# Optimization experiments

Hardware: AMD Instinct MI355X
Metric: run time of the kernel (lower is better)

The kernel has to match this reference:

```python
import jax, jax.numpy as jnp
import numpy as np

N = 3072
F_IN = 512
H1 = 256
HFC = 64
OUT_DIM = 16
NUM_POOL = 3
P_CUT = 30.0  # ps[0]: percentile threshold on positive attention entries
CC_ITERS = 16  # min-label propagation w/ pointer jumping; reach >= 2^16 hops


def l2norm(x):
    # torch F.normalize(p=2, dim=1)
    return x / jnp.clip(jnp.linalg.norm(x, axis=1, keepdims=True), 1e-12, None)


def gcn(x, adj, W, b):
    # standard Kipf GraphConvolution: adj @ (x @ W) + b
    return adj @ (x @ W) + b


def normalize_adj(adj, k):
    n = adj.shape[0]
    A = adj + k * jnp.eye(n, dtype=adj.dtype)
    D = jnp.sqrt(A.sum(0))
    return A / (D[:, None] * D[None, :])


def edge_score(x, adj, a, W, b):
    h = x @ W + b                               # (n, HFC)
    s1 = h @ a[:HFC]                            # (n,)
    s2 = h @ a[HFC:]
    e = jax.nn.sigmoid(s1[:, None] + s2[None, :])
    att = jnp.where(adj > 0, e, jnp.zeros((), e.dtype))
    att = 0.5 * (att + att.T)
    i = jnp.arange(att.shape[0])
    return att.at[i, i].set(1.0)


def percentile_pos(att, p):
    # np.percentile(att[att>0], p) with linear interpolation, jit-safe
    pos = att > 0
    n_pos = pos.sum()
    s = jnp.sort(jnp.where(pos, att, jnp.inf).ravel())
    idx = (n_pos - 1).astype(att.dtype) * (p / 100.0)
    lo = jnp.floor(idx).astype(jnp.int32)
    hi = jnp.ceil(idx).astype(jnp.int32)
    frac = idx - lo.astype(att.dtype)
    return s[lo] * (1.0 - frac) + s[hi] * frac


def cc_labels(mask):
    # connected components via min-label propagation + pointer jumping.
    # diag of mask is always True (att diag = 1), so every node has a neighbor.
    n = mask.shape[0]
    def step(labels, _):
        neigh = jnp.min(jnp.where(mask, labels[None, :], n), axis=1)
        new = jnp.minimum(labels, neigh)
        new = new[new]  # pointer jumping doubles reach each iter
        return new, None
    labels, _ = jax.lax.scan(step, jnp.arange(n, dtype=jnp.int32), None, length=CC_ITERS)
    return labels


def pool(x, adj, att, p):
    cut = percentile_pos(att, p)
    att = att * (att >= cut).astype(att.dtype)
    labels = jax.lax.stop_gradient(cc_labels(att > 0))
    # fixed-shape membership: cluster id = representative (min) node index, padded to N
    C = jax.nn.one_hot(labels, att.shape[0], dtype=x.dtype).T  # (n_clusters=n, n)
    a2 = C @ adj @ C.T
    a2 = 0.5 * (a2 + a2.T)
    cnt = (att > 0).sum(1).astype(x.dtype)  # >=1 since diag survives the cut
    x2 = C @ ((att / cnt[:, None]) @ x)
    return x2, a2, C


def forward(x, adjC, adj, encW0, encb0, encW, encb, fcW, fcb, aW, decW, decb, decW_out, decb_out):
    adjs = [adj]
    adjCs = [adjC]
    xs, Cs, atts = [], [], []
    # ----- encode -----
    for k in range(NUM_POOL):
        x1 = x
        W, b = (encW0, encb0) if k == 0 else (encW[k - 1], encb[k - 1])
        h = jax.nn.relu(gcn(x, adjCs[-1], W, b))
        x = l2norm(h) if k == 0 else l2norm(h + x1)  # residual added for layer idx > 0
        xs.append(x)
        att = edge_score(x, adjs[-1], aW[k], fcW[k], fcb[k])
        x, adjk, C = pool(x, adjs[-1], att, P_CUT)
        adjCk = normalize_adj(adjk, 1.0)  # pool's adjC output is discarded in the original
        x = l2norm(x)
        adjs.append(adjk)
        adjCs.append(adjCk)
        atts.append(att)
        Cs.append(C)
    x = l2norm(jax.nn.elu(gcn(x, adjCs[-1], encW[NUM_POOL - 1], encb[NUM_POOL - 1])))
    xs.append(x)
    # ----- decode -----
    for k in range(NUM_POOL):
        lev = NUM_POOL - k - 1
        x = Cs[lev].T @ x                       # unpool; C is already binary
        x = jnp.concatenate([x, xs[lev]], axis=1)
        x = l2norm(jax.nn.elu(gcn(x, adjCs[lev], decW[k], decb[k])))
    x = gcn(x, adjCs[0], decW_out, decb_out)
    logp = jax.nn.log_softmax(x, axis=1)
    return logp, jnp.stack(Cs), jnp.stack(atts)


def setup_inputs() -> dict:
    key = jax.random.key(0)
    ks = jax.random.split(key, 12)
    x = jax.random.normal(ks[0], (N, F_IN), jnp.float32)
    u = jax.random.uniform(ks[1], (N, N))
    m = (u < 16.0 / N).astype(jnp.float32)  # avg degree ~16
    adj = jnp.maximum(m, m.T)
    i = jnp.arange(N)
    adj = adj.at[i, i].set(1.0)
    adjC = normalize_adj(adj, 1.0)

    def xav(k, shape):
        fan_in = shape[-2] if len(shape) > 1 else shape[-1]
        return jax.random.normal(k, shape, jnp.float32) * (1.0 / np.sqrt(fan_in))

    return {
        "x": x, "adjC": adjC, "adj": adj,
        "encW0": xav(ks[2], (F_IN, H1)), "encb0": jnp.zeros((H1,), jnp.float32),
        "encW": xav(ks[3], (NUM_POOL, H1, H1)), "encb": jnp.zeros((NUM_POOL, H1), jnp.float32),
        "fcW": xav(ks[4], (NUM_POOL, H1, HFC)), "fcb": jnp.zeros((NUM_POOL, HFC), jnp.float32),
        "aW": xav(ks[5], (NUM_POOL, 2 * HFC)),
        "decW": xav(ks[6], (NUM_POOL, 2 * H1, H1)), "decb": jnp.zeros((NUM_POOL, H1), jnp.float32),
        "decW_out": xav(ks[7], (H1, OUT_DIM)), "decb_out": jnp.zeros((OUT_DIM,), jnp.float32),
    }


def reference(x, adjC, adj, encW0, encb0, encW, encb, fcW, fcb, aW, decW, decb, decW_out, decb_out):
    return forward(x, adjC, adj, encW0, encb0, encW, encb, fcW, fcb, aW, decW, decb, decW_out, decb_out)
```

## Files before the change

kernel.cpp:

```cpp
#include <hip/hip_runtime.h>
#include <math.h>

#define NN 3072
#define FF 256
#define CAPE (1<<18)
#define MAXCH 3200

struct Scal {
  int nnzS, nnz2, nzero, mtot, ncht;
  int lo, hi, rank_rem, below_acc, c_le;
  unsigned prefix, vlo, minabove;
  float frac, cut;
};

__device__ __forceinline__ float sigm(float x){ return 1.0f/(1.0f+expf(-x)); }

__global__ __launch_bounds__(256) void k_count_dense(const float* __restrict__ A, int* __restrict__ rowcnt, float* __restrict__ Drow){
  int i=blockIdx.x, t=threadIdx.x;
  int c=0; float sm=0.f;
  for(int j=t;j<NN;j+=256){ float a=A[(size_t)i*NN+j]; if(a!=0.0f||j==i) c++; sm+=a; }
  __shared__ int s[256]; __shared__ float fs[256];
  s[t]=c; fs[t]=sm; __syncthreads();
  for(int o=128;o;o>>=1){ if(t<o){ s[t]+=s[t+o]; fs[t]+=fs[t+o]; } __syncthreads(); }
  if(t==0){ rowcnt[i]=s[0]; if(Drow) Drow[i]=sqrtf(fs[0]+1.0f); }
}

__global__ __launch_bounds__(1024) void k_scan(const int* __restrict__ cnt, int* __restrict__ rp, int* __restrict__ total){
  int t=threadIdx.x;
  int a0=cnt[t*3+0], a1=cnt[t*3+1], a2=cnt[t*3+2];
  int loc=a0+a1+a2;
  __shared__ int s[1024];
  s[t]=loc; __syncthreads();
  for(int o=1;o<1024;o<<=1){ int v=(t>=o)?s[t-o]:0; __syncthreads(); s[t]+=v; __syncthreads(); }
  int excl=s[t]-loc;
  rp[t*3+0]=excl; rp[t*3+1]=excl+a0; rp[t*3+2]=excl+a0+a1;
  if(t==1023){ rp[NN]=s[t]; *total=s[t]; }
}

__global__ __launch_bounds__(256) void k_fill_dense(const float* __restrict__ A, const float* __restrict__ ACd, const float* __restrict__ D,
    const int* __restrict__ rp, int* __restrict__ rows, int* __restrict__ cols, float* __restrict__ aval, float* __restrict__ acval){
  int i=blockIdx.x, t=threadIdx.x;
  const int CH=NN/256;
  int j0=t*CH; int c=0;
  for(int u=0;u<CH;u++){ int j=j0+u; float a=A[(size_t)i*NN+j]; if(a!=0.0f||j==i) c++; }
  __shared__ int s[256]; s[t]=c; __syncthreads();
  for(int o=1;o<256;o<<=1){ int v=(t>=o)?s[t-o]:0; __syncthreads(); s[t]+=v; __syncthreads(); }
  int pos=rp[i]+s[t]-c;
  float Di = D?D[i]:0.0f;
  for(int u=0;u<CH;u++){ int j=j0+u; float a=A[(size_t)i*NN+j];
    if(a!=0.0f||j==i){
      if(pos<CAPE){
        rows[pos]=i; cols[pos]=j; aval[pos]=a;
        acval[pos]= ACd? ACd[(size_t)i*NN+j] : (a+(j==i?1.0f:0.0f))/(Di*D[j]);
      }
      pos++;
    }
  }
}

__global__ __launch_bounds__(256) void k_gemm(const float* __restrict__ A, const float* __restrict__ B, float* __restrict__ C,
                                              int M, int K, int Nc){
  __shared__ float As[16][68];
  __shared__ float Bs[16][68];
  int tid=threadIdx.x;
  int tx=tid&15, ty=tid>>4;
  int bm=blockIdx.y*64, bn=blockIdx.x*64;
  int lm=tid>>2, lk=(tid&3)*4;
  int kr=tid>>4, nf=(tid&15)*4;
  float acc[4][4]={};
  for(int k0=0;k0<K;k0+=16){
    float4 a4=*(const float4*)(A+(size_t)(bm+lm)*K+k0+lk);
    As[lk+0][lm]=a4.x; As[lk+1][lm]=a4.y; As[lk+2][lm]=a4.z; As[lk+3][lm]=a4.w;
    float4 b4=*(const float4*)(B+(size_t)(k0+kr)*Nc+bn+nf);
    *(float4*)&Bs[kr][nf]=b4;
    __syncthreads();
#pragma unroll
    for(int kk=0;kk<16;kk++){
      float4 av=*(const float4*)&As[kk][ty*4];
      float4 bv=*(const float4*)&Bs[kk][tx*4];
      float am[4]={av.x,av.y,av.z,av.w};
      float bb[4]={bv.x,bv.y,bv.z,bv.w};
#pragma unroll
      for(int i2=0;i2<4;i2++)
#pragma unroll
        for(int j2=0;j2<4;j2++) acc[i2][j2]+=am[i2]*bb[j2];
    }
    __syncthreads();
  }
  for(int i2=0;i2<4;i2++){
    float4 o=make_float4(acc[i2][0],acc[i2][1],acc[i2][2],acc[i2][3]);
    *(float4*)(C+(size_t)(bm+ty*4+i2)*Nc+bn+tx*4)=o;
  }
}

__global__ __launch_bounds__(256) void k_gemm16(const float* __restrict__ X, const float* __restrict__ W, float* __restrict__ T){
  int idx=blockIdx.x*256+threadIdx.x;
  if(idx>=NN*16) return;
  int i=idx>>4, o=idx&15;
  float s=0.f;
  for(int kk=0;kk<FF;kk++) s+=X[(size_t)i*FF+kk]*W[kk*16+o];
  T[idx]=s;
}

__global__ __launch_bounds__(256) void k_spmm_gcn(const int* __restrict__ rp, const int* __restrict__ cols, const float* __restrict__ vals,
    const float* __restrict__ X, const float* __restrict__ bias, const float* __restrict__ resid, float* __restrict__ out, int act){
  int wid=blockIdx.x*4+(threadIdx.x>>6);
  int lane=threadIdx.x&63;
  if(wid>=NN) return;
  int e0=rp[wid], e1=rp[wid+1];
  float4 acc=make_float4(0,0,0,0);
  for(int e=e0;e<e1;e++){
    float v=vals[e]; int c=cols[e];
    float4 xv=*(const float4*)(X+(size_t)c*FF+lane*4);
    acc.x+=v*xv.x; acc.y+=v*xv.y; acc.z+=v*xv.z; acc.w+=v*xv.w;
  }
  float4 bv=*(const float4*)(bias+lane*4);
  acc.x+=bv.x; acc.y+=bv.y; acc.z+=bv.z; acc.w+=bv.w;
  if(act==0){
    acc.x=fmaxf(acc.x,0.f); acc.y=fmaxf(acc.y,0.f); acc.z=fmaxf(acc.z,0.f); acc.w=fmaxf(acc.w,0.f);
  } else {
    acc.x=acc.x>0.f?acc.x:expm1f(acc.x); acc.y=acc.y>0.f?acc.y:expm1f(acc.y);
    acc.z=acc.z>0.f?acc.z:expm1f(acc.z); acc.w=acc.w>0.f?acc.w:expm1f(acc.w);
  }
  if(resid){
    float4 r=*(const float4*)(resid+(size_t)wid*FF+lane*4);
    acc.x+=r.x; acc.y+=r.y; acc.z+=r.z; acc.w+=r.w;
  }
  float ss=acc.x*acc.x+acc.y*acc.y+acc.z*acc.z+acc.w*acc.w;
  for(int o=32;o;o>>=1) ss+=__shfl_xor(ss,o);
  float nrm=fmaxf(sqrtf(ss),1e-12f);
  float4 o4=make_float4(acc.x/nrm,acc.y/nrm,acc.z/nrm,acc.w/nrm);
  *(float4*)(out+(size_t)wid*FF+lane*4)=o4;
}

__global__ __launch_bounds__(256) void k_spmm_plain(const int* __restrict__ rp, const int* __restrict__ cols, const float* __restrict__ vals,
    const float* __restrict__ X, float* __restrict__ out){
  int wid=blockIdx.x*4+(threadIdx.x>>6);
  int lane=threadIdx.x&63;
  if(wid>=NN) return;
  int e0=rp[wid], e1=rp[wid+1];
  float4 acc=make_float4(0,0,0,0);
  for(int e=e0;e<e1;e++){
    if(e>=CAPE) break;
    float v=vals[e]; int c=cols[e];
    float4 xv=*(const float4*)(X+(size_t)c*FF+lane*4);
    acc.x+=v*xv.x; acc.y+=v*xv.y; acc.z+=v*xv.z; acc.w+=v*xv.w;
  }
  *(float4*)(out+(size_t)wid*FF+lane*4)=acc;
}

__global__ __launch_bounds__(64) void k_edge(const float* __restrict__ X, const float* __restrict__ fw, const float* __restrict__ fb,
    const float* __restrict__ av, float* __restrict__ s1, float* __restrict__ s2, Scal* sc){
  int i=blockIdx.x, l=threadIdx.x;
  if(i==0&&l==0) sc->nzero=0;
  __shared__ float xr[FF];
  *(float4*)&xr[l*4]=*(const float4*)(X+(size_t)i*FF+l*4);
  __syncthreads();
  float h=fb[l];
  for(int kk=0;kk<FF;kk++) h+=xr[kk]*fw[kk*64+l];
  float p1=h*av[l], p2=h*av[64+l];
  for(int o=32;o;o>>=1){ p1+=__shfl_xor(p1,o); p2+=__shfl_xor(p2,o); }
  if(l==0){ s1[i]=p1; s2[i]=p2; }
}

__global__ __launch_bounds__(256) void k_att_row(const int* __restrict__ rp, const int* __restrict__ cols,
    const float* __restrict__ s1, const float* __restrict__ s2, float* __restrict__ attD, float* __restrict__ cand, Scal* sc){
  __shared__ float row[NN];
  __shared__ int wred[4];
  int i=blockIdx.x, t=threadIdx.x;
  for(int j=t;j<NN;j+=256) row[j]=0.f;
  __syncthreads();
  int e0=rp[i], e1=rp[i+1];
  float s1i=s1[i], s2i=s2[i];
  int nz=0;
  for(int e=e0+t;e<e1;e+=256){
    int j=cols[e];
    float v=(j==i)?1.0f:0.5f*(sigm(s1i+s2[j])+sigm(s1[j]+s2i));
    row[j]=v;
    if(e<CAPE) cand[e]=v;
    if(!(v>0.f)) nz++;
  }
  for(int o=32;o;o>>=1) nz+=__shfl_xor(nz,o);
  if((t&63)==0) wred[t>>6]=nz;
  __syncthreads();
  if(t==0){ int s=wred[0]+wred[1]+wred[2]+wred[3]; if(s) atomicAdd(&sc->nzero,s); }
  float* orow=attD+(size_t)i*NN;
  for(int j=t*4;j<NN;j+=1024) *(float4*)(orow+j)=*(const float4*)&row[j];
}

__global__ void k_prep(Scal* sc){
  int np=sc->nnzS - sc->nzero;
  float idx=(float)(np-1)*(30.0f/100.0f);
  float fl=floorf(idx), ce=ceilf(idx);
  sc->lo=(int)fl; sc->hi=(int)ce; sc->frac=idx-fl;
  sc->rank_rem=sc->lo;
  sc->below_acc=0;
  sc->minabove=0xFFFFFFFFu;
}

template<int PHASE>
__global__ __launch_bounds__(256) void k_hist(const float* __restrict__ cand, const Scal* __restrict__ sc, unsigned* __restrict__ bins){
  const int NB = (PHASE==0)?16384:256;
  __shared__ unsigned h[NB];
  int t=threadIdx.x;
  for(int b=t;b<NB;b+=256) h[b]=0;
  __syncthreads();
  int n=sc->nnzS; if(n>CAPE) n=CAPE;
  unsigned pref=sc->prefix;
  int stride=gridDim.x*256;
  for(int e=blockIdx.x*256+t; e<n; e+=stride){
    float v=cand[e];
    if(!(v>0.f)) continue;
    unsigned bb=__float_as_uint(v);
    if(PHASE==0) atomicAdd(&h[bb>>16],1u);
    else if(PHASE==1){ if((bb>>16)==pref) atomicAdd(&h[(bb>>8)&0xFFu],1u); }
    else { if((bb>>8)==pref) atomicAdd(&h[bb&0xFFu],1u); }
  }
  __syncthreads();
  for(int b=t;b<NB;b+=256){ unsigned c=h[b]; if(c) atomicAdd(&bins[b],c); }
}

template<int PHASE>
__global__ __launch_bounds__(256) void k_pick(const unsigned* __restrict__ bins, Scal* sc){
  const int NB=(PHASE==0)?16384:256;
  const int PER=NB/256;
  __shared__ int part[256];
  __shared__ int selbin; __shared__ int below_sel;
  int t=threadIdx.x;
  int b0=t*PER;
  int sum=0;
  for(int u=0;u<PER;u++) sum+=(int)bins[b0+u];
  part[t]=sum; __syncthreads();
  for(int o=1;o<256;o<<=1){ int v=(t>=o)?part[t-o]:0; __syncthreads(); part[t]+=v; __syncthreads(); }
  int incl=part[t], excl=incl-sum;
  int r=sc->rank_rem;
  if(r>=excl && r<incl){
    int run=excl;
    for(int u=0;u<PER;u++){
      int c=(int)bins[b0+u];
      if(r<run+c){ selbin=b0+u; below_sel=run; break; }
      run+=c;
    }
  }
  __syncthreads();
  if(t==0){
    sc->rank_rem=r-below_sel;
    sc->below_acc+=below_sel;
    if(PHASE==0) sc->prefix=(unsigned)selbin;
    else if(PHASE==1) sc->prefix=(sc->prefix<<8)|(unsigned)selbin;
    else{
      sc->vlo=(sc->prefix<<8)|(unsigned)selbin;
      sc->c_le=sc->below_acc+(int)bins[selbin];
    }
  }
}

__global__ __launch_bounds__(256) void k_minabove(const float* __restrict__ cand, Scal* sc){
  int n=sc->nnzS; if(n>CAPE) n=CAPE;
  unsigned vlo=sc->vlo;
  int tid=threadIdx.x, lane=tid&63;
  int stride=gridDim.x*256;
  for(int base=blockIdx.x*256; base<n; base+=stride){
    int e=base+tid;
    unsigned b=0xFFFFFFFFu;
    if(e<n){ float v=cand[e]; if(v>0.f){ unsigned bb=__float_as_uint(v); if(bb>vlo) b=bb; } }
    for(int o=32;o;o>>=1){ unsigned ob=__shfl_xor(b,o); b=ob<b?ob:b; }
    if(lane==0&&b!=0xFFFFFFFFu) atomicMin(&sc->minabove,b);
  }
}

__global__ void k_cut(Scal* sc){
  float slo=__uint_as_float(sc->vlo);
  float shi;
  if(sc->hi==sc->lo) shi=slo;
  else if(sc->c_le>sc->hi) shi=slo;
  else shi=__uint_as_float(sc->minabove);
  sc->cut=slo*(1.0f-sc->frac)+shi*sc->frac;
}

__global__ __launch_bounds__(256) void k_pc_count(const int* __restrict__ rp, const float* __restrict__ cand, const Scal* __restrict__ sc,
    int* __restrict__ rowcnt, float* __restrict__ cntf){
  int wid=blockIdx.x*4+(threadIdx.x>>6);
  int lane=threadIdx.x&63;
  if(wid>=NN) return;
  int e0=rp[wid], e1=rp[wid+1];
  float cut=sc->cut;
  int c=0;
  for(int e=e0+lane;e<e1;e+=64){ if(e<CAPE && cand[e]>=cut) c++; }
  for(int o=32;o;o>>=1) c+=__shfl_xor(c,o);
  if(lane==0){ rowcnt[wid]=c; cntf[wid]=(float)c; }
}

__global__ __launch_bounds__(256) void k_pc_fill(const int* __restrict__ rp, const int* __restrict__ cols, const float* __restrict__ cand,
    const Scal* __restrict__ sc, const int* __restrict__ rp2, int* __restrict__ rows2, int* __restrict__ cols2, float* __restrict__ pval,
    const float* __restrict__ cntf){
  int wid=blockIdx.x*4+(threadIdx.x>>6);
  int lane=threadIdx.x&63;
  if(wid>=NN) return;
  int e0=rp[wid], e1=rp[wid+1];
  float cut=sc->cut, cf=cntf[wid];
  int base=rp2[wid];
  for(int eb=e0;eb<e1;eb+=64){
    int e=eb+lane;
    bool p=(e<e1)&&(e<CAPE)&&(cand[e]>=cut);
    unsigned long long m=__ballot(p);
    if(p){
      int pos=base+__popcll(m&((1ull<<lane)-1ull));
      if(pos<CAPE){ rows2[pos]=wid; cols2[pos]=cols[e]; pval[pos]=cand[e]/cf; }
    }
    base+=__popcll(m);
  }
}

__global__ __launch_bounds__(1024) void k_cc(const int* __restrict__ rows2, const int* __restrict__ cols2, Scal* sc,
    int* __restrict__ labk, int* __restrict__ moff_g, int* __restrict__ memb,
    int* __restrict__ choff_g, int* __restrict__ chm0_g, int* __restrict__ chm1_g){
  __shared__ int lab[NN];
  __shared__ int cnt[NN];
  __shared__ int mof[NN];
  __shared__ int s[1024];
  __shared__ int chg;
  int t=threadIdx.x;
  for(int i=t;i<NN;i+=1024){ lab[i]=i; cnt[i]=0; }
  int n2=sc->nnz2; if(n2>CAPE) n2=CAPE;
  __syncthreads();
  for(int it=0;it<16;it++){
    if(t==0) chg=0;
    __syncthreads();
    for(int e=t;e<n2;e+=1024){
      int i=rows2[e], j=cols2[e];
      if(i!=j){
        int li=lab[i], lj=lab[j];
        if(lj<li){ if(atomicMin(&lab[i],lj)>lj) chg=1; }
        else if(li<lj){ if(atomicMin(&lab[j],li)>li) chg=1; }
      }
    }
    __syncthreads();
    int l0=lab[t], l1=lab[t+1024], l2=lab[t+2048];
    int v0=lab[l0], v1=lab[l1], v2=lab[l2];
    __syncthreads();
    if(v0<l0){ lab[t]=v0; chg=1; }
    if(v1<l1){ lab[t+1024]=v1; chg=1; }
    if(v2<l2){ lab[t+2048]=v2; chg=1; }
    __syncthreads();
    if(!chg) break;
    __syncthreads();
  }
  for(int i=t;i<NN;i+=1024){ int l=lab[i]; labk[i]=l; atomicAdd(&cnt[l],1); }
  __syncthreads();
  int a0=cnt[t*3+0], a1=cnt[t*3+1], a2=cnt[t*3+2];
  int loc=a0+a1+a2;
  s[t]=loc; __syncthreads();
  for(int o=1;o<1024;o<<=1){ int v=(t>=o)?s[t-o]:0; __syncthreads(); s[t]+=v; __syncthreads(); }
  int excl=s[t]-loc;
  __syncthreads();
  mof[t*3+0]=excl; mof[t*3+1]=excl+a0; mof[t*3+2]=excl+a0+a1;
  cnt[t*3+0]=excl; cnt[t*3+1]=excl+a0; cnt[t*3+2]=excl+a0+a1;
  moff_g[t*3+0]=excl; moff_g[t*3+1]=excl+a0; moff_g[t*3+2]=excl+a0+a1;
  if(t==1023) moff_g[NN]=s[t];
  __syncthreads();
  int ch0=(a0+63)>>6, ch1=(a1+63)>>6, ch2=(a2+63)>>6;
  int locc=ch0+ch1+ch2;
  s[t]=locc; __syncthreads();
  for(int o=1;o<1024;o<<=1){ int v=(t>=o)?s[t-o]:0; __syncthreads(); s[t]+=v; __syncthreads(); }
  int cexcl=s[t]-locc;
  choff_g[t*3+0]=cexcl; choff_g[t*3+1]=cexcl+ch0; choff_g[t*3+2]=cexcl+ch0+ch1;
  if(t==1023){ choff_g[NN]=s[t]; sc->ncht=s[t]; }
  {
    int bases[3]={cexcl,cexcl+ch0,cexcl+ch0+ch1};
    int cnts[3]={a0,a1,a2};
    int nqs[3]={ch0,ch1,ch2};
    for(int u=0;u<3;u++){
      int m0=mof[t*3+u];
      int me=m0+cnts[u];
      for(int q=0;q<nqs[u];q++){
        int idx=bases[u]+q;
        if(idx<MAXCH){
          chm0_g[idx]=m0+q*64;
          int e2=m0+q*64+64; chm1_g[idx]=e2<me?e2:me;
        }
      }
    }
  }
  __syncthreads();
  int lane=t&63, wv=t>>6;
  for(int b=0;b<3;b++){
    int j=b*1024+t;
    int myl=lab[j];
    int rank_w=0,total=0;
#pragma unroll
    for(int l=0;l<64;l++){
      int lb=__shfl(myl,l);
      if(lb==myl){ total++; if(l<lane) rank_w++; }
    }
    for(int w=0;w<16;w++){
      if(wv==w){
        int base=cnt[myl];
        memb[base+rank_w]=j;
        if(rank_w==0) cnt[myl]=base+total;
      }
      __syncthreads();
    }
  }
}

__global__ __launch_bounds__(256) void k_a2e(const int* __restrict__ rowsA, const int* __restrict__ colsA_, const float* __restrict__ aval,
    const Scal* __restrict__ sc, const int* __restrict__ labk, float* __restrict__ dense){
  int e=blockIdx.x*256+threadIdx.x;
  int n=sc->nnzS; if(n>CAPE) n=CAPE;
  int lane=threadIdx.x&63;
  bool valid=(e<n);
  float a=valid?aval[e]:0.f;
  valid=valid&&(a!=0.f);
  int key=0;
  if(valid) key=labk[rowsA[e]]*NN+labk[colsA_[e]];
  unsigned long long act=__ballot(valid);
  while(act){
    int leader=__ffsll(act)-1;
    int lkey=__shfl(key,leader);
    bool same=valid&&(key==lkey);
    float contrib=same?a:0.f;
    for(int o=32;o;o>>=1) contrib+=__shfl_xor(contrib,o);
    if(lane==leader) atomicAdd(&dense[(size_t)lkey],contrib);
    act&=~__ballot(same);
  }
}

__global__ __launch_bounds__(256) void k_x2p(const float* __restrict__ y, const int* __restrict__ memb,
    const int* __restrict__ chm0, const int* __restrict__ chm1, const Scal* __restrict__ sc, float* __restrict__ partial){
  int b=blockIdx.x;
  if(b>=sc->ncht||b>=MAXCH) return;
  int t=threadIdx.x;
  int m0=chm0[b], m1=chm1[b];
  float acc=0.f;
#pragma unroll 4
  for(int m=m0;m<m1;m++) acc+=y[(size_t)memb[m]*FF+t];
  partial[(size_t)b*FF+t]=acc;
}
__global__ __launch_bounds__(256) void k_x2f(const int* __restrict__ choff, const float* __restrict__ partial, float* __restrict__ out){
  int c=blockIdx.x, t=threadIdx.x;
  int q0=choff[c], q1=choff[c+1];
  float acc=0.f;
  for(int q=q0;q<q1&&q<MAXCH;q++) acc+=partial[(size_t)q*FF+t];
  __shared__ float red[256];
  red[t]=acc*acc; __syncthreads();
  for(int o=128;o;o>>=1){ if(t<o) red[t]+=red[t+o]; __syncthreads(); }
  float nrm=fmaxf(sqrtf(red[0]),1e-12f);
  out[(size_t)c*FF+t]=(q1>q0)?acc/nrm:0.f;
}

__global__ __launch_bounds__(256) void k_gather(const float* __restrict__ X, const int* __restrict__ labs, const float* __restrict__ xsk,
    float* __restrict__ xcat){
  int idx=blockIdx.x*256+threadIdx.x;
  if(idx>=NN*128) return;
  int j=idx>>7, f4=idx&127;
  float4 v;
  if(f4<64) v=*(const float4*)(X+(size_t)labs[j]*FF+f4*4);
  else v=*(const float4*)(xsk+(size_t)j*FF+(size_t)(f4-64)*4);
  *(float4*)(xcat+(size_t)j*512+(size_t)f4*4)=v;
}

__global__ __launch_bounds__(256) void k_final(const int* __restrict__ rp, const int* __restrict__ cols, const float* __restrict__ vals,
    const float* __restrict__ T, const float* __restrict__ bias, float* __restrict__ logp){
  int i=blockIdx.x*256+threadIdx.x;
  if(i>=NN) return;
  float o[16];
#pragma unroll
  for(int f=0;f<16;f++) o[f]=bias[f];
  int e1=rp[i+1];
  for(int e=rp[i];e<e1;e++){
    float v=vals[e]; const float* tr=T+(size_t)cols[e]*16;
#pragma unroll
    for(int f=0;f<16;f++) o[f]+=v*tr[f];
  }
  float m=o[0];
#pragma unroll
  for(int f=1;f<16;f++) m=fmaxf(m,o[f]);
  float ssum=0.f;
#pragma unroll
  for(int f=0;f<16;f++) ssum+=expf(o[f]-m);
  float lse=logf(ssum);
#pragma unroll
  for(int f=0;f<16;f++) logp[(size_t)i*16+f]=o[f]-m-lse;
}

__global__ __launch_bounds__(256) void k_cfill(const int* __restrict__ labsv, float* __restrict__ CsB){
  int idx=blockIdx.x*256+threadIdx.x;
  if(idx>=3*NN) return;
  int l=idx/NN, j=idx-l*NN;
  int c=labsv[l*NN+j];
  CsB[(size_t)l*NN*NN+(size_t)c*NN+j]=1.0f;
}

extern "C" void kernel_launch(void* const* d_in, const int* in_sizes, int n_in,
                              void* d_out, int out_size, void* d_ws, size_t ws_size,
                              hipStream_t stream) {
  (void)in_sizes; (void)n_in; (void)out_size;
  const float* x_in =(const float*)d_in[0];
  const float* adjC =(const float*)d_in[1];
  const float* adj  =(const float*)d_in[2];
  const float* encW0=(const float*)d_in[3];
  const float* encb0=(const float*)d_in[4];
  const float* encW =(const float*)d_in[5];
  const float* encb =(const float*)d_in[6];
  const float* fcW  =(const float*)d_in[7];
  const float* fcb  =(const float*)d_in[8];
  const float* aW   =(const float*)d_in[9];
  const float* decW =(const float*)d_in[10];
  const float* decb =(const float*)d_in[11];
  const float* decWo=(const float*)d_in[12];
  const float* decbo=(const float*)d_in[13];
  float* out=(float*)d_out;

  float* logp=out;
  float* CsB = out + (size_t)NN*16;
  float* attB= CsB + 3ull*NN*NN;
  float* slot1 = CsB + (size_t)NN*NN;
  float* xs[4]; for(int i=0;i<4;i++) xs[i]=slot1+(size_t)i*NN*FF;
  float* xcur=slot1+(size_t)4*NN*FF;
  float* ybuf=slot1+(size_t)5*NN*FF;
  float* tbuf=slot1+(size_t)6*NN*FF;
  float* slot2 = CsB + 2ull*NN*NN;
  float* xcat=slot2;
  float* t16 = xcat + (size_t)NN*512;

  char* w=(char*)d_ws; size_t off=0;
  auto alc=[&](size_t b)->void*{ off=(off+255)&~(size_t)255; void* r=w+off; off+=b; return r; };
  Scal* sc=(Scal*)alc(sizeof(Scal));
  int* rowcnt=(int*)alc((size_t)NN*4);
  int* rp[4]; for(int i=0;i<4;i++) rp[i]=(int*)alc((size_t)(NN+1)*4);
  int* rp2=(int*)alc((size_t)(NN+1)*4);
  int* colsA[4]; float* acv[4];
  for(int i=0;i<4;i++){ colsA[i]=(int*)alc((size_t)CAPE*4); acv[i]=(float*)alc((size_t)CAPE*4); }
  float* avalS=(float*)alc((size_t)CAPE*4);
  int* rowsA=(int*)alc((size_t)CAPE*4);
  float* cand=(float*)alc((size_t)CAPE*4);
  int* rows2=(int*)alc((size_t)CAPE*4);
  int* cols2=(int*)alc((size_t)CAPE*4);
  float* pval=(float*)alc((size_t)CAPE*4);
  unsigned* bins=(unsigned*)alc((size_t)16384*4);
  int* labsv=(int*)alc((size_t)3*NN*4);
  int* moff=(int*)alc((size_t)(NN+1)*4);
  int* memb=(int*)alc((size_t)NN*4);
  int* choff=(int*)alc((size_t)(NN+1)*4);
  int* chm0=(int*)alc((size_t)MAXCH*4);
  int* chm1=(int*)alc((size_t)MAXCH*4);
  float* partial=(float*)alc((size_t)MAXCH*FF*4);
  float* cntf=(float*)alc((size_t)NN*4);
  float* s1=(float*)alc((size_t)NN*4);
  float* s2v=(float*)alc((size_t)NN*4);
  float* Dv=(float*)alc((size_t)NN*4);
  float* dense;
  size_t denseB=(size_t)NN*NN*4;
  if(ws_size>=off+denseB+4096) dense=(float*)alc(denseB);
  else dense=CsB;

  auto build_csr=[&](const float* Ad, const float* ACd, const float* Dp, int lvl){
    k_count_dense<<<NN,256,0,stream>>>(Ad,rowcnt,Dv);
    k_scan<<<1,1024,0,stream>>>(rowcnt,rp[lvl],&sc->nnzS);
    k_fill_dense<<<NN,256,0,stream>>>(Ad,ACd,Dp,rp[lvl],rowsA,colsA[lvl],avalS,acv[lvl]);
  };

  build_csr(adj,adjC,nullptr,0);

  for(int k=0;k<3;k++){
    const float* xin=(k==0)?x_in:xcur;
    const float* Wk=(k==0)?encW0:(encW+(size_t)(k-1)*FF*FF);
    const float* bk=(k==0)?encb0:(encb+(size_t)(k-1)*FF);
    int K=(k==0)?512:FF;
    k_gemm<<<dim3(FF/64,NN/64),256,0,stream>>>(xin,Wk,tbuf,NN,K,FF);
    k_spmm_gcn<<<NN/4,256,0,stream>>>(rp[k],colsA[k],acv[k],tbuf,bk,(k==0)?nullptr:xcur,xs[k],0);

    k_edge<<<NN,64,0,stream>>>(xs[k],fcW+(size_t)k*FF*64,fcb+(size_t)k*64,aW+(size_t)k*128,s1,s2v,sc);
    k_att_row<<<NN,256,0,stream>>>(rp[k],colsA[k],s1,s2v,attB+(size_t)k*NN*NN,cand,sc);

    k_prep<<<1,1,0,stream>>>(sc);
    hipMemsetAsync(bins,0,(size_t)16384*4,stream);
    k_hist<0><<<64,256,0,stream>>>(cand,sc,bins);
    k_pick<0><<<1,256,0,stream>>>(bins,sc);
    hipMemsetAsync(bins,0,(size_t)256*4,stream);
    k_hist<1><<<64,256,0,stream>>>(cand,sc,bins);
    k_pick<1><<<1,256,0,stream>>>(bins,sc);
    hipMemsetAsync(bins,0,(size_t)256*4,stream);
    k_hist<2><<<64,256,0,stream>>>(cand,sc,bins);
    k_pick<2><<<1,256,0,stream>>>(bins,sc);
    k_minabove<<<256,256,0,stream>>>(cand,sc);
    k_cut<<<1,1,0,stream>>>(sc);

    k_pc_count<<<NN/4,256,0,stream>>>(rp[k],cand,sc,rowcnt,cntf);
    k_scan<<<1,1024,0,stream>>>(rowcnt,rp2,&sc->nnz2);
    k_pc_fill<<<NN/4,256,0,stream>>>(rp[k],colsA[k],cand,sc,rp2,rows2,cols2,pval,cntf);

    k_cc<<<1,1024,0,stream>>>(rows2,cols2,sc,labsv+(size_t)k*NN,moff,memb,choff,chm0,chm1);

    hipMemsetAsync(dense,0,denseB,stream);
    k_a2e<<<CAPE/256,256,0,stream>>>(rowsA,colsA[k],avalS,sc,labsv+(size_t)k*NN,dense);

    k_spmm_plain<<<NN/4,256,0,stream>>>(rp2,cols2,pval,xs[k],ybuf);
    k_x2p<<<MAXCH,256,0,stream>>>(ybuf,memb,chm0,chm1,sc,partial);
    k_x2f<<<NN,256,0,stream>>>(choff,partial,xcur);

    build_csr(dense,nullptr,Dv,k+1);
  }

  k_gemm<<<dim3(FF/64,NN/64),256,0,stream>>>(xcur,encW+(size_t)2*FF*FF,tbuf,NN,FF,FF);
  k_spmm_gcn<<<NN/4,256,0,stream>>>(rp[3],colsA[3],acv[3],tbuf,encb+(size_t)2*FF,nullptr,xs[3],1);

  float* xd=xs[3];
  float* outsb[3]={xcur,ybuf,xcur};
  for(int k=0;k<3;k++){
    int lev=2-k;
    k_gather<<<(NN*128)/256,256,0,stream>>>(xd,labsv+(size_t)lev*NN,xs[lev],xcat);
    k_gemm<<<dim3(FF/64,NN/64),256,0,stream>>>(xcat,decW+(size_t)k*512*FF,tbuf,NN,512,FF);
    k_spmm_gcn<<<NN/4,256,0,stream>>>(rp[lev],colsA[lev],acv[lev],tbuf,decb+(size_t)k*FF,nullptr,outsb[k],1);
    xd=outsb[k];
  }

  k_gemm16<<<(NN*16)/256,256,0,stream>>>(xd,decWo,t16);
  k_final<<<(NN+255)/256,256,0,stream>>>(rp[0],colsA[0],acv[0],t16,decbo,logp);

  hipMemsetAsync(CsB,0,3ull*NN*NN*4,stream);
  k_cfill<<<(3*NN+255)/256,256,0,stream>>>(labsv,CsB);
}
```

Measured before the change: 915.7 us.

## Fuse CSR build and percentile selection into fewer kernels with atomic row offsets

Replaces the count/scan/fill sequence with single-pass CSR builders that keep the dense row in registers and claim row offsets via atomicAdd, storing per-row start and length instead of a prefix-sum row pointer. The three-pass radix percentile select becomes one 16-bit histogram, a ballot-based collection of candidates in the selected bin, and a single-block finish kernel. The prune count and fill are merged into one atomic-offset kernel, and normalized adjacency values are computed on the fly from degree vectors in the GCN SpMM. The aim is to drop many small launches, memsets and a second dense read; in exchange rows become non-contiguous in CSR order, which may hurt locality and could alter behaviour of code that assumes row-ordered edges.

```diff
diff --git a/kernel.cpp b/kernel.cpp
--- a/kernel.cpp
+++ b/kernel.cpp
@@ -7,52 +7,63 @@
 #define MAXCH 3200
 
 struct Scal {
-  int nnzS, nnz2, nzero, mtot, ncht;
-  int lo, hi, rank_rem, below_acc, c_le;
-  unsigned prefix, vlo, minabove;
+  int nnzS, nnz2, nzero, ncht, ccount;
+  int lo, hi, rank_rem, below_acc;
+  unsigned prefix, minabove;
   float frac, cut;
 };
 
 __device__ __forceinline__ float sigm(float x){ return 1.0f/(1.0f+expf(-x)); }
 
-__global__ __launch_bounds__(256) void k_count_dense(const float* __restrict__ A, int* __restrict__ rowcnt, float* __restrict__ Drow){
-  int i=blockIdx.x, t=threadIdx.x;
-  int c=0; float sm=0.f;
-  for(int j=t;j<NN;j+=256){ float a=A[(size_t)i*NN+j]; if(a!=0.0f||j==i) c++; sm+=a; }
-  __shared__ int s[256]; __shared__ float fs[256];
-  s[t]=c; fs[t]=sm; __syncthreads();
-  for(int o=128;o;o>>=1){ if(t<o){ s[t]+=s[t+o]; fs[t]+=fs[t+o]; } __syncthreads(); }
-  if(t==0){ rowcnt[i]=s[0]; if(Drow) Drow[i]=sqrtf(fs[0]+1.0f); }
-}
-
-__global__ __launch_bounds__(1024) void k_scan(const int* __restrict__ cnt, int* __restrict__ rp, int* __restrict__ total){
-  int t=threadIdx.x;
-  int a0=cnt[t*3+0], a1=cnt[t*3+1], a2=cnt[t*3+2];
-  int loc=a0+a1+a2;
-  __shared__ int s[1024];
-  s[t]=loc; __syncthreads();
-  for(int o=1;o<1024;o<<=1){ int v=(t>=o)?s[t-o]:0; __syncthreads(); s[t]+=v; __syncthreads(); }
-  int excl=s[t]-loc;
-  rp[t*3+0]=excl; rp[t*3+1]=excl+a0; rp[t*3+2]=excl+a0+a1;
-  if(t==1023){ rp[NN]=s[t]; *total=s[t]; }
-}
-
-__global__ __launch_bounds__(256) void k_fill_dense(const float* __restrict__ A, const float* __restrict__ ACd, const float* __restrict__ D,
-    const int* __restrict__ rp, int* __restrict__ rows, int* __restrict__ cols, float* __restrict__ aval, float* __restrict__ acval){
+__global__ __launch_bounds__(256) void k_init(unsigned* __restrict__ bins, Scal* sc){
+  int i=blockIdx.x*256+threadIdx.x;
+  if(i<16384) bins[i]=0;
+  if(i==0){ sc->nnzS=0; sc->nzero=0; sc->nnz2=0; sc->ccount=0; sc->minabove=0xFFFFFFFFu; }
+}
+
+__global__ __launch_bounds__(256) void k_csr0(const float* __restrict__ A, const float* __restrict__ ACd,
+    int* __restrict__ rs, int* __restrict__ rl, int* __restrict__ rows, int* __restrict__ cols,
+    float* __restrict__ aval, float* __restrict__ acv, Scal* sc){
   int i=blockIdx.x, t=threadIdx.x;
   const int CH=NN/256;
   int j0=t*CH; int c=0;
-  for(int u=0;u<CH;u++){ int j=j0+u; float a=A[(size_t)i*NN+j]; if(a!=0.0f||j==i) c++; }
-  __shared__ int s[256]; s[t]=c; __syncthreads();
+  float av[CH];
+  for(int u=0;u<CH;u++){ int j=j0+u; float a=A[(size_t)i*NN+j]; av[u]=a; if(a!=0.0f||j==i) c++; }
+  __shared__ int s[256]; __shared__ int sbase;
+  s[t]=c; __syncthreads();
   for(int o=1;o<256;o<<=1){ int v=(t>=o)?s[t-o]:0; __syncthreads(); s[t]+=v; __syncthreads(); }
-  int pos=rp[i]+s[t]-c;
-  float Di = D?D[i]:0.0f;
-  for(int u=0;u<CH;u++){ int j=j0+u; float a=A[(size_t)i*NN+j];
+  if(t==255){ int total=s[255]; sbase=atomicAdd(&sc->nnzS,total); rl[i]=total; }
+  __syncthreads();
+  int base=sbase;
+  if(t==0) rs[i]=base;
+  int pos=base+s[t]-c;
+  for(int u=0;u<CH;u++){ int j=j0+u; float a=av[u];
     if(a!=0.0f||j==i){
-      if(pos<CAPE){
-        rows[pos]=i; cols[pos]=j; aval[pos]=a;
-        acval[pos]= ACd? ACd[(size_t)i*NN+j] : (a+(j==i?1.0f:0.0f))/(Di*D[j]);
-      }
+      if(pos<CAPE){ rows[pos]=i; cols[pos]=j; aval[pos]=a; acv[pos]=ACd[(size_t)i*NN+j]; }
+      pos++;
+    }
+  }
+}
+
+__global__ __launch_bounds__(256) void k_csrP(const float* __restrict__ A,
+    int* __restrict__ rs, int* __restrict__ rl, int* __restrict__ rows, int* __restrict__ cols,
+    float* __restrict__ aval, float* __restrict__ Drow, Scal* sc){
+  int i=blockIdx.x, t=threadIdx.x;
+  const int CH=NN/256;
+  int j0=t*CH; int c=0; float sm=0.f;
+  float av[CH];
+  for(int u=0;u<CH;u++){ int j=j0+u; float a=A[(size_t)i*NN+j]; av[u]=a; sm+=a; if(a!=0.0f||j==i) c++; }
+  __shared__ int s[256]; __shared__ float fs[256]; __shared__ int sbase;
+  s[t]=c; fs[t]=sm; __syncthreads();
+  for(int o=1;o<256;o<<=1){ int v=(t>=o)?s[t-o]:0; float f=(t>=o)?fs[t-o]:0.f; __syncthreads(); s[t]+=v; fs[t]+=f; __syncthreads(); }
+  if(t==255){ int total=s[255]; sbase=atomicAdd(&sc->nnzS,total); rl[i]=total; Drow[i]=sqrtf(fs[255]+1.0f); }
+  __syncthreads();
+  int base=sbase;
+  if(t==0) rs[i]=base;
+  int pos=base+s[t]-c;
+  for(int u=0;u<CH;u++){ int j=j0+u; float a=av[u];
+    if(a!=0.0f||j==i){
+      if(pos<CAPE){ rows[pos]=i; cols[pos]=j; aval[pos]=a; }
       pos++;
     }
   }
@@ -76,10 +87,10 @@
     __syncthreads();
 #pragma unroll
     for(int kk=0;kk<16;kk++){
-      float4 av=*(const float4*)&As[kk][ty*4];
-      float4 bv=*(const float4*)&Bs[kk][tx*4];
-      float am[4]={av.x,av.y,av.z,av.w};
-      float bb[4]={bv.x,bv.y,bv.z,bv.w};
+      float4 avv=*(const float4*)&As[kk][ty*4];
+      float4 bvv=*(const float4*)&Bs[kk][tx*4];
+      float am[4]={avv.x,avv.y,avv.z,avv.w};
+      float bb[4]={bvv.x,bvv.y,bvv.z,bvv.w};
 #pragma unroll
       for(int i2=0;i2<4;i2++)
 #pragma unroll
@@ -102,15 +113,20 @@
   T[idx]=s;
 }
 
-__global__ __launch_bounds__(256) void k_spmm_gcn(const int* __restrict__ rp, const int* __restrict__ cols, const float* __restrict__ vals,
-    const float* __restrict__ X, const float* __restrict__ bias, const float* __restrict__ resid, float* __restrict__ out, int act){
+__global__ __launch_bounds__(256) void k_spmm_gcn(const int* __restrict__ rs, const int* __restrict__ rl,
+    const int* __restrict__ cols, const float* __restrict__ vals, const float* __restrict__ D,
+    const float* __restrict__ X, const float* __restrict__ bias, const float* __restrict__ resid,
+    float* __restrict__ out, int act){
   int wid=blockIdx.x*4+(threadIdx.x>>6);
   int lane=threadIdx.x&63;
   if(wid>=NN) return;
-  int e0=rp[wid], e1=rp[wid+1];
+  int e0=rs[wid], e1=e0+rl[wid];
+  float di=D?D[wid]:1.0f;
   float4 acc=make_float4(0,0,0,0);
   for(int e=e0;e<e1;e++){
+    if(e>=CAPE) break;
     float v=vals[e]; int c=cols[e];
+    if(D) v=(v+(c==wid?1.0f:0.0f))/(di*D[c]);
     float4 xv=*(const float4*)(X+(size_t)c*FF+lane*4);
     acc.x+=v*xv.x; acc.y+=v*xv.y; acc.z+=v*xv.z; acc.w+=v*xv.w;
   }
@@ -133,12 +149,12 @@
   *(float4*)(out+(size_t)wid*FF+lane*4)=o4;
 }
 
-__global__ __launch_bounds__(256) void k_spmm_plain(const int* __restrict__ rp, const int* __restrict__ cols, const float* __restrict__ vals,
-    const float* __restrict__ X, float* __restrict__ out){
+__global__ __launch_bounds__(256) void k_spmm_plain(const int* __restrict__ rs, const int* __restrict__ rl,
+    const int* __restrict__ cols, const float* __restrict__ vals, const float* __restrict__ X, float* __restrict__ out){
   int wid=blockIdx.x*4+(threadIdx.x>>6);
   int lane=threadIdx.x&63;
   if(wid>=NN) return;
-  int e0=rp[wid], e1=rp[wid+1];
+  int e0=rs[wid], e1=e0+rl[wid];
   float4 acc=make_float4(0,0,0,0);
   for(int e=e0;e<e1;e++){
     if(e>=CAPE) break;
@@ -163,21 +179,22 @@
   if(l==0){ s1[i]=p1; s2[i]=p2; }
 }
 
-__global__ __launch_bounds__(256) void k_att_row(const int* __restrict__ rp, const int* __restrict__ cols,
+__global__ __launch_bounds__(256) void k_att_row(const int* __restrict__ rs, const int* __restrict__ rl, const int* __restrict__ cols,
     const float* __restrict__ s1, const float* __restrict__ s2, float* __restrict__ attD, float* __restrict__ cand, Scal* sc){
   __shared__ float row[NN];
   __shared__ int wred[4];
   int i=blockIdx.x, t=threadIdx.x;
   for(int j=t;j<NN;j+=256) row[j]=0.f;
   __syncthreads();
-  int e0=rp[i], e1=rp[i+1];
+  int e0=rs[i], e1=e0+rl[i];
   float s1i=s1[i], s2i=s2[i];
   int nz=0;
   for(int e=e0+t;e<e1;e+=256){
+    if(e>=CAPE) break;
     int j=cols[e];
     float v=(j==i)?1.0f:0.5f*(sigm(s1i+s2[j])+sigm(s1[j]+s2i));
     row[j]=v;
-    if(e<CAPE) cand[e]=v;
+    cand[e]=v;
     if(!(v>0.f)) nz++;
   }
   for(int o=32;o;o>>=1) nz+=__shfl_xor(nz,o);
@@ -188,55 +205,44 @@
   for(int j=t*4;j<NN;j+=1024) *(float4*)(orow+j)=*(const float4*)&row[j];
 }
 
-__global__ void k_prep(Scal* sc){
-  int np=sc->nnzS - sc->nzero;
-  float idx=(float)(np-1)*(30.0f/100.0f);
-  float fl=floorf(idx), ce=ceilf(idx);
-  sc->lo=(int)fl; sc->hi=(int)ce; sc->frac=idx-fl;
-  sc->rank_rem=sc->lo;
-  sc->below_acc=0;
-  sc->minabove=0xFFFFFFFFu;
-}
-
-template<int PHASE>
-__global__ __launch_bounds__(256) void k_hist(const float* __restrict__ cand, const Scal* __restrict__ sc, unsigned* __restrict__ bins){
-  const int NB = (PHASE==0)?16384:256;
-  __shared__ unsigned h[NB];
+__global__ __launch_bounds__(256) void k_hist14(const float* __restrict__ cand, const Scal* __restrict__ sc, unsigned* __restrict__ bins){
+  __shared__ unsigned h[16384];
   int t=threadIdx.x;
-  for(int b=t;b<NB;b+=256) h[b]=0;
+  for(int b=t;b<16384;b+=256) h[b]=0;
   __syncthreads();
   int n=sc->nnzS; if(n>CAPE) n=CAPE;
-  unsigned pref=sc->prefix;
   int stride=gridDim.x*256;
   for(int e=blockIdx.x*256+t; e<n; e+=stride){
     float v=cand[e];
-    if(!(v>0.f)) continue;
-    unsigned bb=__float_as_uint(v);
-    if(PHASE==0) atomicAdd(&h[bb>>16],1u);
-    else if(PHASE==1){ if((bb>>16)==pref) atomicAdd(&h[(bb>>8)&0xFFu],1u); }
-    else { if((bb>>8)==pref) atomicAdd(&h[bb&0xFFu],1u); }
-  }
-  __syncthreads();
-  for(int b=t;b<NB;b+=256){ unsigned c=h[b]; if(c) atomicAdd(&bins[b],c); }
-}
-
-template<int PHASE>
-__global__ __launch_bounds__(256) void k_pick(const unsigned* __restrict__ bins, Scal* sc){
-  const int NB=(PHASE==0)?16384:256;
-  const int PER=NB/256;
+    if(v>0.f) atomicAdd(&h[__float_as_uint(v)>>16],1u);
+  }
+  __syncthreads();
+  for(int b=t;b<16384;b+=256){ unsigned c=h[b]; if(c) atomicAdd(&bins[b],c); }
+}
+
+__global__ __launch_bounds__(256) void k_pick14(unsigned* __restrict__ bins, Scal* sc){
   __shared__ int part[256];
-  __shared__ int selbin; __shared__ int below_sel;
+  __shared__ int selbin; __shared__ int below_sel; __shared__ int sh_r;
   int t=threadIdx.x;
-  int b0=t*PER;
+  if(t==0){
+    int np=sc->nnzS - sc->nzero;
+    float idx=(float)(np-1)*(30.0f/100.0f);
+    float fl=floorf(idx), ce=ceilf(idx);
+    sc->lo=(int)fl; sc->hi=(int)ce; sc->frac=idx-fl;
+    sc->ccount=0; sc->minabove=0xFFFFFFFFu;
+    sh_r=(int)fl;
+  }
+  __syncthreads();
+  int r=sh_r;
+  int b0=t*64;
   int sum=0;
-  for(int u=0;u<PER;u++) sum+=(int)bins[b0+u];
+  for(int u=0;u<64;u++) sum+=(int)bins[b0+u];
   part[t]=sum; __syncthreads();
   for(int o=1;o<256;o<<=1){ int v=(t>=o)?part[t-o]:0; __syncthreads(); part[t]+=v; __syncthreads(); }
   int incl=part[t], excl=incl-sum;
-  int r=sc->rank_rem;
   if(r>=excl && r<incl){
     int run=excl;
-    for(int u=0;u<PER;u++){
+    for(int u=0;u<64;u++){
       int c=(int)bins[b0+u];
       if(r<run+c){ selbin=b0+u; below_sel=run; break; }
       run+=c;
@@ -245,61 +251,109 @@
   __syncthreads();
   if(t==0){
     sc->rank_rem=r-below_sel;
-    sc->below_acc+=below_sel;
-    if(PHASE==0) sc->prefix=(unsigned)selbin;
-    else if(PHASE==1) sc->prefix=(sc->prefix<<8)|(unsigned)selbin;
-    else{
-      sc->vlo=(sc->prefix<<8)|(unsigned)selbin;
-      sc->c_le=sc->below_acc+(int)bins[selbin];
-    }
-  }
-}
-
-__global__ __launch_bounds__(256) void k_minabove(const float* __restrict__ cand, Scal* sc){
+    sc->below_acc=below_sel;
+    sc->prefix=(unsigned)selbin;
+  }
+  for(int b=t;b<16384;b+=256) bins[b]=0;
+}
+
+__global__ __launch_bounds__(256) void k_collect(const float* __restrict__ cand, Scal* sc, unsigned* __restrict__ collbuf){
   int n=sc->nnzS; if(n>CAPE) n=CAPE;
-  unsigned vlo=sc->vlo;
+  unsigned pref=sc->prefix;
   int tid=threadIdx.x, lane=tid&63;
   int stride=gridDim.x*256;
   for(int base=blockIdx.x*256; base<n; base+=stride){
     int e=base+tid;
-    unsigned b=0xFFFFFFFFu;
-    if(e<n){ float v=cand[e]; if(v>0.f){ unsigned bb=__float_as_uint(v); if(bb>vlo) b=bb; } }
-    for(int o=32;o;o>>=1){ unsigned ob=__shfl_xor(b,o); b=ob<b?ob:b; }
-    if(lane==0&&b!=0xFFFFFFFFu) atomicMin(&sc->minabove,b);
-  }
-}
-
-__global__ void k_cut(Scal* sc){
-  float slo=__uint_as_float(sc->vlo);
-  float shi;
-  if(sc->hi==sc->lo) shi=slo;
-  else if(sc->c_le>sc->hi) shi=slo;
-  else shi=__uint_as_float(sc->minabove);
-  sc->cut=slo*(1.0f-sc->frac)+shi*sc->frac;
-}
-
-__global__ __launch_bounds__(256) void k_pc_count(const int* __restrict__ rp, const float* __restrict__ cand, const Scal* __restrict__ sc,
-    int* __restrict__ rowcnt, float* __restrict__ cntf){
+    unsigned bb=0; bool inb=false; unsigned above=0xFFFFFFFFu;
+    if(e<n){
+      float v=cand[e];
+      if(v>0.f){
+        bb=__float_as_uint(v);
+        unsigned key=bb>>16;
+        if(key==pref) inb=true;
+        else if(key>pref) above=bb;
+      }
+    }
+    unsigned long long bal=__ballot(inb);
+    if(bal){
+      int leader=__ffsll(bal)-1;
+      int cnt=__popcll(bal);
+      int wbase=0;
+      if(lane==leader) wbase=atomicAdd(&sc->ccount,cnt);
+      wbase=__shfl(wbase,leader);
+      if(inb){
+        int rk=__popcll(bal&((1ull<<lane)-1ull));
+        if(wbase+rk<CAPE) collbuf[wbase+rk]=bb;
+      }
+    }
+    for(int o=32;o;o>>=1){ unsigned ob=__shfl_xor(above,o); above=ob<above?ob:above; }
+    if(lane==0&&above!=0xFFFFFFFFu) atomicMin(&sc->minabove,above);
+  }
+}
+
+__global__ __launch_bounds__(1024) void k_sel2(const unsigned* __restrict__ collbuf, Scal* sc){
+  __shared__ unsigned h[256];
+  __shared__ int sel1, below1, sel2, below2, cnt2;
+  __shared__ unsigned red[1024];
+  int t=threadIdx.x;
+  int n=sc->ccount; if(n>CAPE) n=CAPE;
+  int r=sc->rank_rem;
+  if(t<256) h[t]=0;
+  __syncthreads();
+  for(int e=t;e<n;e+=1024) atomicAdd(&h[(collbuf[e]>>8)&0xFFu],1u);
+  __syncthreads();
+  if(t==0){
+    int run=0;
+    for(int b=0;b<256;b++){ int c=(int)h[b]; if(r<run+c){ sel1=b; below1=run; break; } run+=c; }
+  }
+  __syncthreads();
+  int s1b=sel1;
+  int r2=r-below1;
+  if(t<256) h[t]=0;
+  __syncthreads();
+  for(int e=t;e<n;e+=1024){ unsigned bb=collbuf[e]; if(((bb>>8)&0xFFu)==(unsigned)s1b) atomicAdd(&h[bb&0xFFu],1u); }
+  __syncthreads();
+  if(t==0){
+    int run=0;
+    for(int b=0;b<256;b++){ int c=(int)h[b]; if(r2<run+c){ sel2=b; below2=run; cnt2=c; break; } run+=c; }
+  }
+  __syncthreads();
+  unsigned vlo=(sc->prefix<<16)|((unsigned)s1b<<8)|(unsigned)sel2;
+  unsigned mn=0xFFFFFFFFu;
+  for(int e=t;e<n;e+=1024){ unsigned bb=collbuf[e]; if(bb>vlo&&bb<mn) mn=bb; }
+  red[t]=mn; __syncthreads();
+  for(int o=512;o;o>>=1){ if(t<o){ unsigned ob=red[t+o]; if(ob<red[t]) red[t]=ob; } __syncthreads(); }
+  if(t==0){
+    unsigned minab=red[0]<sc->minabove?red[0]:sc->minabove;
+    int c_le=sc->below_acc+below1+below2+cnt2;
+    float slo=__uint_as_float(vlo);
+    float shi;
+    if(sc->hi==sc->lo) shi=slo;
+    else if(c_le>sc->hi) shi=slo;
+    else shi=__uint_as_float(minab);
+    sc->cut=slo*(1.0f-sc->frac)+shi*sc->frac;
+    sc->nnz2=0;
+  }
+}
+
+__global__ __launch_bounds__(256) void k_pc(const int* __restrict__ rs, const int* __restrict__ rl, const int* __restrict__ cols,
+    const float* __restrict__ cand, Scal* sc, int* __restrict__ rs2, int* __restrict__ rl2,
+    int* __restrict__ rows2, int* __restrict__ cols2, float* __restrict__ pval, float* __restrict__ cntf){
   int wid=blockIdx.x*4+(threadIdx.x>>6);
   int lane=threadIdx.x&63;
   if(wid>=NN) return;
-  int e0=rp[wid], e1=rp[wid+1];
+  int e0=rs[wid], e1=e0+rl[wid];
   float cut=sc->cut;
   int c=0;
   for(int e=e0+lane;e<e1;e+=64){ if(e<CAPE && cand[e]>=cut) c++; }
   for(int o=32;o;o>>=1) c+=__shfl_xor(c,o);
-  if(lane==0){ rowcnt[wid]=c; cntf[wid]=(float)c; }
-}
-
-__global__ __launch_bounds__(256) void k_pc_fill(const int* __restrict__ rp, const int* __restrict__ cols, const float* __restrict__ cand,
-    const Scal* __restrict__ sc, const int* __restrict__ rp2, int* __restrict__ rows2, int* __restrict__ cols2, float* __restrict__ pval,
-    const float* __restrict__ cntf){
-  int wid=blockIdx.x*4+(threadIdx.x>>6);
-  int lane=threadIdx.x&63;
-  if(wid>=NN) return;
-  int e0=rp[wid], e1=rp[wid+1];
-  float cut=sc->cut, cf=cntf[wid];
-  int base=rp2[wid];
+  int base=0;
+  if(lane==0){
+    base=atomicAdd(&sc->nnz2,c);
+    rs2[wid]=base; rl2[wid]=c; cntf[wid]=(float)c;
+  }
+  base=__shfl(base,0);
+  float cf=(float)c;
   for(int eb=e0;eb<e1;eb+=64){
     int e=eb+lane;
     bool p=(e<e1)&&(e<CAPE)&&(cand[e]>=cut);
@@ -437,8 +491,9 @@
   for(int m=m0;m<m1;m++) acc+=y[(size_t)memb[m]*FF+t];
   partial[(size_t)b*FF+t]=acc;
 }
-__global__ __launch_bounds__(256) void k_x2f(const int* __restrict__ choff, const float* __restrict__ partial, float* __restrict__ out){
+__global__ __launch_bounds__(256) void k_x2f(const int* __restrict__ choff, const float* __restrict__ partial, float* __restrict__ out, Scal* sc){
   int c=blockIdx.x, t=threadIdx.x;
+  if(c==0&&t==0) sc->nnzS=0;
   int q0=choff[c], q1=choff[c+1];
   float acc=0.f;
   for(int q=q0;q<q1&&q<MAXCH;q++) acc+=partial[(size_t)q*FF+t];
@@ -460,15 +515,16 @@
   *(float4*)(xcat+(size_t)j*512+(size_t)f4*4)=v;
 }
 
-__global__ __launch_bounds__(256) void k_final(const int* __restrict__ rp, const int* __restrict__ cols, const float* __restrict__ vals,
-    const float* __restrict__ T, const float* __restrict__ bias, float* __restrict__ logp){
+__global__ __launch_bounds__(256) void k_final(const int* __restrict__ rs, const int* __restrict__ rl, const int* __restrict__ cols,
+    const float* __restrict__ vals, const float* __restrict__ T, const float* __restrict__ bias, float* __restrict__ logp){
   int i=blockIdx.x*256+threadIdx.x;
   if(i>=NN) return;
   float o[16];
 #pragma unroll
   for(int f=0;f<16;f++) o[f]=bias[f];
-  int e1=rp[i+1];
-  for(int e=rp[i];e<e1;e++){
+  int e0=rs[i], e1=e0+rl[i];
+  for(int e=e0;e<e1;e++){
+    if(e>=CAPE) break;
     float v=vals[e]; const float* tr=T+(size_t)cols[e]*16;
 #pragma unroll
     for(int f=0;f<16;f++) o[f]+=v*tr[f];
@@ -527,14 +583,18 @@
   char* w=(char*)d_ws; size_t off=0;
   auto alc=[&](size_t b)->void*{ off=(off+255)&~(size_t)255; void* r=w+off; off+=b; return r; };
   Scal* sc=(Scal*)alc(sizeof(Scal));
-  int* rowcnt=(int*)alc((size_t)NN*4);
-  int* rp[4]; for(int i=0;i<4;i++) rp[i]=(int*)alc((size_t)(NN+1)*4);
-  int* rp2=(int*)alc((size_t)(NN+1)*4);
-  int* colsA[4]; float* acv[4];
-  for(int i=0;i<4;i++){ colsA[i]=(int*)alc((size_t)CAPE*4); acv[i]=(float*)alc((size_t)CAPE*4); }
-  float* avalS=(float*)alc((size_t)CAPE*4);
+  int* rsL[4]; int* rlL[4]; int* colsA[4]; float* avalA[4]; float* DL[4];
+  for(int i=0;i<4;i++){
+    rsL[i]=(int*)alc((size_t)NN*4); rlL[i]=(int*)alc((size_t)NN*4);
+    colsA[i]=(int*)alc((size_t)CAPE*4); avalA[i]=(float*)alc((size_t)CAPE*4);
+    DL[i]=(float*)alc((size_t)NN*4);
+  }
+  float* acv0=(float*)alc((size_t)CAPE*4);
   int* rowsA=(int*)alc((size_t)CAPE*4);
   float* cand=(float*)alc((size_t)CAPE*4);
+  unsigned* collbuf=(unsigned*)alc((size_t)CAPE*4);
+  int* rs2=(int*)alc((size_t)NN*4);
+  int* rl2=(int*)alc((size_t)NN*4);
   int* rows2=(int*)alc((size_t)CAPE*4);
   int* cols2=(int*)alc((size_t)CAPE*4);
   float* pval=(float*)alc((size_t)CAPE*4);
@@ -549,19 +609,13 @@
   float* cntf=(float*)alc((size_t)NN*4);
   float* s1=(float*)alc((size_t)NN*4);
   float* s2v=(float*)alc((size_t)NN*4);
-  float* Dv=(float*)alc((size_t)NN*4);
   float* dense;
   size_t denseB=(size_t)NN*NN*4;
   if(ws_size>=off+denseB+4096) dense=(float*)alc(denseB);
   else dense=CsB;
 
-  auto build_csr=[&](const float* Ad, const float* ACd, const float* Dp, int lvl){
-    k_count_dense<<<NN,256,0,stream>>>(Ad,rowcnt,Dv);
-    k_scan<<<1,1024,0,stream>>>(rowcnt,rp[lvl],&sc->nnzS);
-    k_fill_dense<<<NN,256,0,stream>>>(Ad,ACd,Dp,rp[lvl],rowsA,colsA[lvl],avalS,acv[lvl]);
-  };
-
-  build_csr(adj,adjC,nullptr,0);
+  k_init<<<64,256,0,stream>>>(bins,sc);
+  k_csr0<<<NN,256,0,stream>>>(adj,adjC,rsL[0],rlL[0],rowsA,colsA[0],avalA[0],acv0,sc);
 
   for(int k=0;k<3;k++){
     const float* xin=(k==0)?x_in:xcur;
@@ -569,42 +623,34 @@
     const float* bk=(k==0)?encb0:(encb+(size_t)(k-1)*FF);
     int K=(k==0)?512:FF;
     k_gemm<<<dim3(FF/64,NN/64),256,0,stream>>>(xin,Wk,tbuf,NN,K,FF);
-    k_spmm_gcn<<<NN/4,256,0,stream>>>(rp[k],colsA[k],acv[k],tbuf,bk,(k==0)?nullptr:xcur,xs[k],0);
+    const float* vk=(k==0)?acv0:avalA[k];
+    const float* Dk=(k==0)?nullptr:DL[k];
+    k_spmm_gcn<<<NN/4,256,0,stream>>>(rsL[k],rlL[k],colsA[k],vk,Dk,tbuf,bk,(k==0)?nullptr:xcur,xs[k],0);
 
     k_edge<<<NN,64,0,stream>>>(xs[k],fcW+(size_t)k*FF*64,fcb+(size_t)k*64,aW+(size_t)k*128,s1,s2v,sc);
-    k_att_row<<<NN,256,0,stream>>>(rp[k],colsA[k],s1,s2v,attB+(size_t)k*NN*NN,cand,sc);
-
-    k_prep<<<1,1,0,stream>>>(sc);
-    hipMemsetAsync(bins,0,(size_t)16384*4,stream);
-    k_hist<0><<<64,256,0,stream>>>(cand,sc,bins);
-    k_pick<0><<<1,256,0,stream>>>(bins,sc);
-    hipMemsetAsync(bins,0,(size_t)256*4,stream);
-    k_hist<1><<<64,256,0,stream>>>(cand,sc,bins);
-    k_pick<1><<<1,256,0,stream>>>(bins,sc);
-    hipMemsetAsync(bins,0,(size_t)256*4,stream);
-    k_hist<2><<<64,256,0,stream>>>(cand,sc,bins);
-    k_pick<2><<<1,256,0,stream>>>(bins,sc);
-    k_minabove<<<256,256,0,stream>>>(cand,sc);
-    k_cut<<<1,1,0,stream>>>(sc);
-
-    k_pc_count<<<NN/4,256,0,stream>>>(rp[k],cand,sc,rowcnt,cntf);
-    k_scan<<<1,1024,0,stream>>>(rowcnt,rp2,&sc->nnz2);
-    k_pc_fill<<<NN/4,256,0,stream>>>(rp[k],colsA[k],cand,sc,rp2,rows2,cols2,pval,cntf);
+    k_att_row<<<NN,256,0,stream>>>(rsL[k],rlL[k],colsA[k],s1,s2v,attB+(size_t)k*NN*NN,cand,sc);
+
+    k_hist14<<<64,256,0,stream>>>(cand,sc,bins);
+    k_pick14<<<1,256,0,stream>>>(bins,sc);
+    k_collect<<<64,256,0,stream>>>(cand,sc,collbuf);
+    k_sel2<<<1,1024,0,stream>>>(collbuf,sc);
+
+    k_pc<<<NN/4,256,0,stream>>>(rsL[k],rlL[k],colsA[k],cand,sc,rs2,rl2,rows2,cols2,pval,cntf);
 
     k_cc<<<1,1024,0,stream>>>(rows2,cols2,sc,labsv+(size_t)k*NN,moff,memb,choff,chm0,chm1);
 
     hipMemsetAsync(dense,0,denseB,stream);
-    k_a2e<<<CAPE/256,256,0,stream>>>(rowsA,colsA[k],avalS,sc,labsv+(size_t)k*NN,dense);
-
-    k_spmm_plain<<<NN/4,256,0,stream>>>(rp2,cols2,pval,xs[k],ybuf);
+    k_a2e<<<CAPE/256,256,0,stream>>>(rowsA,colsA[k],avalA[k],sc,labsv+(size_t)k*NN,dense);
+
+    k_spmm_plain<<<NN/4,256,0,stream>>>(rs2,rl2,cols2,pval,xs[k],ybuf);
     k_x2p<<<MAXCH,256,0,stream>>>(ybuf,memb,chm0,chm1,sc,partial);
-    k_x2f<<<NN,256,0,stream>>>(choff,partial,xcur);
-
-    build_csr(dense,nullptr,Dv,k+1);
+    k_x2f<<<NN,256,0,stream>>>(choff,partial,xcur,sc);
+
+    k_csrP<<<NN,256,0,stream>>>(dense,rsL[k+1],rlL[k+1],rowsA,colsA[k+1],avalA[k+1],DL[k+1],sc);
   }
 
   k_gemm<<<dim3(FF/64,NN/64),256,0,stream>>>(xcur,encW+(size_t)2*FF*FF,tbuf,NN,FF,FF);
-  k_spmm_gcn<<<NN/4,256,0,stream>>>(rp[3],colsA[3],acv[3],tbuf,encb+(size_t)2*FF,nullptr,xs[3],1);
+  k_spmm_gcn<<<NN/4,256,0,stream>>>(rsL[3],rlL[3],colsA[3],avalA[3],DL[3],tbuf,encb+(size_t)2*FF,nullptr,xs[3],1);
 
   float* xd=xs[3];
   float* outsb[3]={xcur,ybuf,xcur};
@@ -612,12 +658,14 @@
     int lev=2-k;
     k_gather<<<(NN*128)/256,256,0,stream>>>(xd,labsv+(size_t)lev*NN,xs[lev],xcat);
     k_gemm<<<dim3(FF/64,NN/64),256,0,stream>>>(xcat,decW+(size_t)k*512*FF,tbuf,NN,512,FF);
-    k_spmm_gcn<<<NN/4,256,0,stream>>>(rp[lev],colsA[lev],acv[lev],tbuf,decb+(size_t)k*FF,nullptr,outsb[k],1);
+    const float* vk=(lev==0)?acv0:avalA[lev];
+    const float* Dk=(lev==0)?nullptr:DL[lev];
+    k_spmm_gcn<<<NN/4,256,0,stream>>>(rsL[lev],rlL[lev],colsA[lev],vk,Dk,tbuf,decb+(size_t)k*FF,nullptr,outsb[k],1);
     xd=outsb[k];
   }
 
   k_gemm16<<<(NN*16)/256,256,0,stream>>>(xd,decWo,t16);
-  k_final<<<(NN+255)/256,256,0,stream>>>(rp[0],colsA[0],acv[0],t16,decbo,logp);
+  k_final<<<(NN+255)/256,256,0,stream>>>(rsL[0],rlL[0],colsA[0],acv0,t16,decbo,logp);
 
   hipMemsetAsync(CsB,0,3ull*NN*NN*4,stream);
   k_cfill<<<(3*NN+255)/256,256,0,stream>>>(labsv,CsB);
```

After: 1.094 ms. 1.19x slower.
